# Kernel tuning notes

Measured on AMD Instinct MI355X. Metric: run time of the kernel, lower is better.

The kernel has to match this reference:

```python
import jax, jax.numpy as jnp
import numpy as np

HIDDEN = 768

def setup_inputs() -> dict:
    key = jax.random.key(0)
    k1, k2, k3 = jax.random.split(key, 3)
    x = jax.random.normal(k1, (8, 2048, HIDDEN), dtype=jnp.float32)
    # nn.Linear(hidden, 3*hidden): weight [3H, H], bias [3H]; torch init ~ U(-1/sqrt(H), 1/sqrt(H))
    bound = 1.0 / np.sqrt(HIDDEN)
    W = jax.random.uniform(k2, (3 * HIDDEN, HIDDEN), dtype=jnp.float32, minval=-bound, maxval=bound)
    b = jax.random.uniform(k3, (3 * HIDDEN,), dtype=jnp.float32, minval=-bound, maxval=bound)
    return {"x": x, "W": W, "b": b}

def reference(x, W, b):
    # qkv: [B, N, 3H]
    qkv = jnp.einsum('bnd,hd->bnh', x, W) + b
    q, k, v = jnp.split(qkv, 3, axis=-1)  # each [B, N, H]
    # NOTE: original module applies NO 1/sqrt(d) scaling — kept faithful.
    weights = jnp.einsum('bnd,bmd->bnm', q, k)          # [B, N, N]
    weights = jax.nn.softmax(weights, axis=-1)
    out = jnp.einsum('bnm,bmd->bnd', weights, v)        # [B, N, H]
    return out
```

## Files before the change

kernel.cpp:

```cpp
#include <hip/hip_runtime.h>


typedef short    s16x8 __attribute__((ext_vector_type(8)));
typedef _Float16 h16x8 __attribute__((ext_vector_type(8)));
typedef _Float16 h16x4 __attribute__((ext_vector_type(4)));
typedef float    f32x4 __attribute__((ext_vector_type(4)));

__device__ __forceinline__ unsigned short f2bf(float x) {
    unsigned u = __float_as_uint(x);
    u += 0x7fffu + ((u >> 16) & 1u);
    return (unsigned short)(u >> 16);
}
__device__ __forceinline__ float bf2f(unsigned short h) {
    return __uint_as_float(((unsigned)h) << 16);
}
__device__ __forceinline__ unsigned short f2h(float x) {
    _Float16 h = (_Float16)x;
    unsigned short u;
    __builtin_memcpy(&u, &h, 2);
    return u;
}

__device__ __forceinline__ void gld16(const void* g, void* l) {
    __builtin_amdgcn_global_load_lds(
        (const __attribute__((address_space(1))) unsigned int*)(unsigned long long)g,
        (__attribute__((address_space(3))) unsigned int*)(unsigned)(unsigned long long)l,
        16, 0, 0);
}

template<int MODE, bool FP16, int SWZ>
__global__ __launch_bounds__(256, 2)
void gemm_mfma(const unsigned short* __restrict__ A, const unsigned short* __restrict__ B,
               const float* __restrict__ bias, const float* __restrict__ rvec,
               float* __restrict__ Cf, unsigned short* __restrict__ Ch,
               int K, int lda, int ldb, int ldc,
               long long sA, long long sB, long long sC, long long sR)
{
    __shared__ unsigned short As[4096];
    __shared__ unsigned short Bs[4096];

    int bx = blockIdx.x, by = blockIdx.y, bz = blockIdx.z;
    if (SWZ == 1) {
        const int l = bx + gridDim.x * (by + gridDim.y * bz);
        bz = l & 7;
        const int t = l >> 3;
        bx = t % gridDim.x;
        by = t / gridDim.x;
    } else if (SWZ == 2) {
        const int l = bx + gridDim.x * by;
        const int c = l & 7;
        const int t = l >> 3;
        const int rows = gridDim.y >> 3;
        bx = t % gridDim.x;
        by = c * rows + t / gridDim.x;
    }

    A += (long long)bz * sA;
    B += (long long)bz * sB;

    const long long m0 = (long long)by * 128;
    const long long n0 = (long long)bx * 128;

    const int tid  = threadIdx.x;
    const int wave = tid >> 6, lane = tid & 63;
    const int rr_  = lane >> 2, kc = (lane & 3) * 8;
    const int wm = (wave & 1) * 64, wn = (wave >> 1) * 64;
    const int ml = lane & 15, kq = (lane >> 4) * 8;

    f32x4 acc[4][4];
#pragma unroll
    for (int i = 0; i < 4; ++i)
#pragma unroll
        for (int j = 0; j < 4; ++j) acc[i][j] = f32x4{0.f, 0.f, 0.f, 0.f};

    for (int kt = 0; kt < K; kt += 32) {
        __syncthreads();
#pragma unroll
        for (int i = 0; i < 2; ++i) {
            const int sc = wave * 2 + i;
            const long long ar = m0 + sc * 16 + rr_;
            const long long br = n0 + sc * 16 + rr_;
            gld16(A + ar * (long long)lda + kt + kc, As + sc * 512);
            gld16(B + br * (long long)ldb + kt + kc, Bs + sc * 512);
        }
        __syncthreads();

#pragma unroll
        for (int i = 0; i < 4; ++i) {
            const int ai = (wm + i * 16 + ml) * 32 + kq;
#pragma unroll
            for (int j = 0; j < 4; ++j) {
                const int bi = (wn + j * 16 + ml) * 32 + kq;
                if (FP16)
                    acc[i][j] = __builtin_amdgcn_mfma_f32_16x16x32_f16(
                        *(const h16x8*)&As[ai], *(const h16x8*)&Bs[bi], acc[i][j], 0, 0, 0);
                else
                    acc[i][j] = __builtin_amdgcn_mfma_f32_16x16x32_bf16(
                        *(const s16x8*)&As[ai], *(const s16x8*)&Bs[bi], acc[i][j], 0, 0, 0);
            }
        }
    }

    const int r0 = (lane >> 4) * 4;
    if (MODE == 1 || MODE == 2) {
#pragma unroll
        for (int i = 0; i < 4; ++i) {
            const long long rowb = m0 + wm + i * 16 + r0;
#pragma unroll
            for (int j = 0; j < 4; ++j) {
                const long long col = n0 + wn + j * 16 + ml;
                const float bj = bias[col];
#pragma unroll
                for (int q = 0; q < 4; ++q) {
                    const float v = acc[i][j][q] + bj;
                    Ch[(rowb + q) * (long long)ldc + col] = (MODE == 1) ? f2h(v) : f2bf(v);
                }
            }
        }
    } else if (MODE == 3) {
        Ch += (long long)bz * sC;
#pragma unroll
        for (int i = 0; i < 4; ++i) {
            const long long rowb = m0 + wm + i * 16 + r0;
#pragma unroll
            for (int j = 0; j < 4; ++j) {
                const long long col = n0 + wn + j * 16 + ml;
#pragma unroll
                for (int q = 0; q < 4; ++q)
                    Ch[(rowb + q) * (long long)ldc + col] = f2bf(__expf(acc[i][j][q]));
            }
        }
    } else {
        Cf += (long long)bz * sC;
        rvec += (long long)bz * sR;
#pragma unroll
        for (int i = 0; i < 4; ++i) {
            const long long rowb = m0 + wm + i * 16 + r0;
#pragma unroll
            for (int j = 0; j < 4; ++j) {
                const long long col = n0 + wn + j * 16 + ml;
#pragma unroll
                for (int q = 0; q < 4; ++q)
                    Cf[(rowb + q) * (long long)ldc + col] = acc[i][j][q] * rvec[rowb + q];
            }
        }
    }
}

__global__ __launch_bounds__(256)
void cvt_f16(const float* __restrict__ in, unsigned short* __restrict__ out, long long n4)
{
    const long long i = (long long)blockIdx.x * 256 + threadIdx.x;
    if (i >= n4) return;
    const float4 v = ((const float4*)in)[i];
    h16x4 o;
    o.x = (_Float16)v.x; o.y = (_Float16)v.y;
    o.z = (_Float16)v.z; o.w = (_Float16)v.w;
    ((h16x4*)out)[i] = o;
}

__global__ __launch_bounds__(256)
void transpose_v(const unsigned short* __restrict__ v, unsigned short* __restrict__ vt)
{
    __shared__ unsigned short t[32][33];
    const int b = blockIdx.z;
    const int n0 = blockIdx.x * 32, h0 = blockIdx.y * 32;
    const int tx = threadIdx.x, ty = threadIdx.y;
    const unsigned short* src = v + (long long)b * 2048 * 768;
#pragma unroll
    for (int q = 0; q < 4; ++q)
        t[ty + q * 8][tx] = src[(long long)(n0 + ty + q * 8) * 768 + h0 + tx];
    __syncthreads();
    unsigned short* dst = vt + ((long long)b * 768 + h0) * 2048 + n0;
#pragma unroll
    for (int q = 0; q < 4; ++q)
        dst[(long long)(ty + q * 8) * 2048 + tx] = t[tx][ty + q * 8];
}

__global__ __launch_bounds__(256)
void rowsum_recip(const unsigned short* __restrict__ E, float* __restrict__ r)
{
    const long long row = blockIdx.x;
    const int t = threadIdx.x, lane = t & 63, w = t >> 6;
    __shared__ float red[4];
    const uint4 v = ((const uint4*)(E + row * 2048))[t];
    float s = bf2f((unsigned short)(v.x & 0xffff)) + bf2f((unsigned short)(v.x >> 16))
            + bf2f((unsigned short)(v.y & 0xffff)) + bf2f((unsigned short)(v.y >> 16))
            + bf2f((unsigned short)(v.z & 0xffff)) + bf2f((unsigned short)(v.z >> 16))
            + bf2f((unsigned short)(v.w & 0xffff)) + bf2f((unsigned short)(v.w >> 16));
#pragma unroll
    for (int o = 32; o; o >>= 1) s += __shfl_xor(s, o);
    if (lane == 0) red[w] = s;
    __syncthreads();
    if (t == 0) r[row] = 1.f / ((red[0] + red[1]) + (red[2] + red[3]));
}

extern "C" void kernel_launch(void* const* d_in, const int* in_sizes, int n_in,
                              void* d_out, int out_size, void* d_ws, size_t ws_size,
                              hipStream_t stream)
{
    const float* x    = (const float*)d_in[0];
    const float* W    = (const float*)d_in[1];
    const float* bias = (const float*)d_in[2];
    float* out = (float*)d_out;

    char* ws = (char*)d_ws;
    unsigned short* xh = (unsigned short*)ws;
    unsigned short* Wh = (unsigned short*)(ws + 25165824LL);
    unsigned short* qk = (unsigned short*)(ws + 28704768LL);
    unsigned short* v  = (unsigned short*)(ws + 79036416LL);
    unsigned short* vt = (unsigned short*)(ws + 104202240LL);
    unsigned short* E  = (unsigned short*)(ws + 129368064LL);
    float*          r  = (float*)(ws + 196476928LL);

    cvt_f16<<<dim3(12288), dim3(256), 0, stream>>>(x, xh, 3145728LL);
    cvt_f16<<<dim3(1728),  dim3(256), 0, stream>>>(W, Wh, 442368LL);

    gemm_mfma<1, true, 2><<<dim3(12, 128, 1), dim3(256), 0, stream>>>(
        xh, Wh, bias, nullptr, nullptr, qk,
        768, 768, 768, 1536, 0, 0, 0, 0);

    gemm_mfma<2, true, 2><<<dim3(6, 128, 1), dim3(256), 0, stream>>>(
        xh, Wh + 1536LL * 768, bias + 1536, nullptr, nullptr, v,
        768, 768, 768, 768, 0, 0, 0, 0);

    transpose_v<<<dim3(64, 24, 8), dim3(32, 8), 0, stream>>>(v, vt);

    gemm_mfma<3, true, 1><<<dim3(16, 16, 8), dim3(256), 0, stream>>>(
        qk, qk + 768, nullptr, nullptr, nullptr, E,
        768, 1536, 1536, 2048,
        2048LL * 1536, 2048LL * 1536, 2048LL * 2048, 0);

    rowsum_recip<<<dim3(16384), dim3(256), 0, stream>>>(E, r);

    gemm_mfma<4, false, 1><<<dim3(6, 16, 8), dim3(256), 0, stream>>>(
        E, vt, nullptr, r, out, nullptr,
        2048, 2048, 2048, 768,
        2048LL * 2048, 768LL * 2048, 2048LL * 768, 2048);
}
```

Baseline: 341.5 us.

## Use 256x256 tiles with 8 waves and a 4-stage LDS prefetch pipeline

Rewrites the MFMA GEMM to compute a 256x256 output tile per 512-thread block, with each wave covering 128x64. Global-to-LDS loads go into a 4-deep ring buffer, prefetched three K-steps ahead, with explicit waitcnt and barriers so the loads overlap the MFMAs. s_setprio is raised around the MFMA bursts. The goal is more operand reuse per LDS load and hidden global latency, at the cost of 128KB of LDS per block and far fewer blocks in the grid, which risks low occupancy and tail underutilisation on the small projection GEMMs.

```diff
diff --git a/kernel.cpp b/kernel.cpp
--- a/kernel.cpp
+++ b/kernel.cpp
@@ -20,6 +20,9 @@
     __builtin_memcpy(&u, &h, 2);
     return u;
 }
+__device__ __forceinline__ h16x8 as_h(s16x8 v) {
+    h16x8 r; __builtin_memcpy(&r, &v, 16); return r;
+}
 
 __device__ __forceinline__ void gld16(const void* g, void* l) {
     __builtin_amdgcn_global_load_lds(
@@ -28,16 +31,24 @@
         16, 0, 0);
 }
 
+template<bool FP16>
+__device__ __forceinline__ f32x4 mma(s16x8 a, s16x8 b, f32x4 c) {
+    if constexpr (FP16)
+        return __builtin_amdgcn_mfma_f32_16x16x32_f16(as_h(a), as_h(b), c, 0, 0, 0);
+    else
+        return __builtin_amdgcn_mfma_f32_16x16x32_bf16(a, b, c, 0, 0, 0);
+}
+
 template<int MODE, bool FP16, int SWZ>
-__global__ __launch_bounds__(256, 2)
+__global__ __launch_bounds__(512, 2)
 void gemm_mfma(const unsigned short* __restrict__ A, const unsigned short* __restrict__ B,
                const float* __restrict__ bias, const float* __restrict__ rvec,
                float* __restrict__ Cf, unsigned short* __restrict__ Ch,
                int K, int lda, int ldb, int ldc,
                long long sA, long long sB, long long sC, long long sR)
 {
-    __shared__ unsigned short As[4096];
-    __shared__ unsigned short Bs[4096];
+    __shared__ unsigned short As[4][8192];
+    __shared__ unsigned short Bs[4][8192];
 
     int bx = blockIdx.x, by = blockIdx.y, bz = blockIdx.z;
     if (SWZ == 1) {
@@ -58,73 +69,119 @@
     A += (long long)bz * sA;
     B += (long long)bz * sB;
 
-    const long long m0 = (long long)by * 128;
-    const long long n0 = (long long)bx * 128;
+    const long long m0 = (long long)by * 256;
+    const long long n0 = (long long)bx * 256;
 
     const int tid  = threadIdx.x;
     const int wave = tid >> 6, lane = tid & 63;
-    const int rr_  = lane >> 2, kc = (lane & 3) * 8;
-    const int wm = (wave & 1) * 64, wn = (wave >> 1) * 64;
+    const int wr = wave >> 2, wc = wave & 3;
     const int ml = lane & 15, kq = (lane >> 4) * 8;
-
-    f32x4 acc[4][4];
-#pragma unroll
-    for (int i = 0; i < 4; ++i)
+    const int srr = wave * 16 + (lane >> 2);
+    const int skc = (lane & 3) * 8;
+
+    const int aidx = (wr * 128 + ml) * 32 + kq;
+    const int bidx = (wc * 64  + ml) * 32 + kq;
+
+    const unsigned short* Abase = A + (m0 + srr) * (long long)lda + skc;
+    const unsigned short* Bbase = B + (n0 + srr) * (long long)ldb + skc;
+    const long long a128 = 128LL * lda, b128 = 128LL * ldb;
+
+    auto stage_a = [&](int t, int buf) {
+        const unsigned short* p = Abase + t * 32;
+        gld16(p,        &As[buf][wave * 512]);
+        gld16(p + a128, &As[buf][4096 + wave * 512]);
+    };
+    auto stage_b = [&](int t, int buf) {
+        const unsigned short* p = Bbase + t * 32;
+        gld16(p,        &Bs[buf][wave * 512]);
+        gld16(p + b128, &Bs[buf][4096 + wave * 512]);
+    };
+
+    f32x4 acc[8][4];
+#pragma unroll
+    for (int i = 0; i < 8; ++i)
 #pragma unroll
         for (int j = 0; j < 4; ++j) acc[i][j] = f32x4{0.f, 0.f, 0.f, 0.f};
 
-    for (int kt = 0; kt < K; kt += 32) {
-        __syncthreads();
-#pragma unroll
-        for (int i = 0; i < 2; ++i) {
-            const int sc = wave * 2 + i;
-            const long long ar = m0 + sc * 16 + rr_;
-            const long long br = n0 + sc * 16 + rr_;
-            gld16(A + ar * (long long)lda + kt + kc, As + sc * 512);
-            gld16(B + br * (long long)ldb + kt + kc, Bs + sc * 512);
-        }
-        __syncthreads();
-
-#pragma unroll
-        for (int i = 0; i < 4; ++i) {
-            const int ai = (wm + i * 16 + ml) * 32 + kq;
+    const int nt = K >> 5;
+
+    stage_a(0, 0); stage_b(0, 0);
+    stage_a(1, 1); stage_b(1, 1);
+    stage_a(2, 2); stage_b(2, 2);
+    asm volatile("s_waitcnt vmcnt(8)");
+    __builtin_amdgcn_s_barrier();
+
+    for (int t = 0; t < nt; ++t) {
+        const int cur = t & 3;
+        const unsigned short* as = &As[cur][0];
+        const unsigned short* bs = &Bs[cur][0];
+        const bool pf = (t + 3 < nt);
+        const int nb = (t + 3) & 3;
+
+        s16x8 a4[4], b4[4];
+
+#pragma unroll
+        for (int i = 0; i < 4; ++i) a4[i] = *(const s16x8*)&as[aidx + i * 512];
+#pragma unroll
+        for (int j = 0; j < 4; ++j) b4[j] = *(const s16x8*)&bs[bidx + j * 512];
+        if (pf) stage_a(t + 3, nb);
+        __builtin_amdgcn_s_barrier();
+        asm volatile("s_waitcnt lgkmcnt(0)");
+        __builtin_amdgcn_sched_barrier(0);
+        __builtin_amdgcn_s_setprio(1);
+#pragma unroll
+        for (int i = 0; i < 4; ++i)
+#pragma unroll
+            for (int j = 0; j < 4; ++j)
+                acc[i][j] = mma<FP16>(a4[i], b4[j], acc[i][j]);
+        __builtin_amdgcn_s_setprio(0);
+        __builtin_amdgcn_s_barrier();
+
+#pragma unroll
+        for (int i = 0; i < 4; ++i) a4[i] = *(const s16x8*)&as[aidx + (i + 4) * 512];
+        if (pf) stage_b(t + 3, nb);
+        __builtin_amdgcn_s_barrier();
+        asm volatile("s_waitcnt lgkmcnt(0)");
+        __builtin_amdgcn_sched_barrier(0);
+        __builtin_amdgcn_s_setprio(1);
+#pragma unroll
+        for (int i = 0; i < 4; ++i)
+#pragma unroll
+            for (int j = 0; j < 4; ++j)
+                acc[i + 4][j] = mma<FP16>(a4[i], b4[j], acc[i + 4][j]);
+        __builtin_amdgcn_s_setprio(0);
+        if (pf)                { asm volatile("s_waitcnt vmcnt(8)"); }
+        else if (t + 3 == nt)  { asm volatile("s_waitcnt vmcnt(4)"); }
+        else if (t + 2 == nt)  { asm volatile("s_waitcnt vmcnt(0)"); }
+        __builtin_amdgcn_s_barrier();
+    }
+
+    const int r0 = (lane >> 4) * 4;
+    const long long rowbase = m0 + wr * 128 + r0;
+    const long long colbase = n0 + wc * 64 + ml;
+    if (MODE == 1 || MODE == 2) {
+#pragma unroll
+        for (int i = 0; i < 8; ++i) {
+            const long long rowb = rowbase + i * 16;
 #pragma unroll
             for (int j = 0; j < 4; ++j) {
-                const int bi = (wn + j * 16 + ml) * 32 + kq;
-                if (FP16)
-                    acc[i][j] = __builtin_amdgcn_mfma_f32_16x16x32_f16(
-                        *(const h16x8*)&As[ai], *(const h16x8*)&Bs[bi], acc[i][j], 0, 0, 0);
-                else
-                    acc[i][j] = __builtin_amdgcn_mfma_f32_16x16x32_bf16(
-                        *(const s16x8*)&As[ai], *(const s16x8*)&Bs[bi], acc[i][j], 0, 0, 0);
-            }
-        }
-    }
-
-    const int r0 = (lane >> 4) * 4;
-    if (MODE == 1 || MODE == 2) {
-#pragma unroll
-        for (int i = 0; i < 4; ++i) {
-            const long long rowb = m0 + wm + i * 16 + r0;
-#pragma unroll
-            for (int j = 0; j < 4; ++j) {
-                const long long col = n0 + wn + j * 16 + ml;
+                const long long col = colbase + j * 16;
                 const float bj = bias[col];
 #pragma unroll
                 for (int q = 0; q < 4; ++q) {
-                    const float v = acc[i][j][q] + bj;
-                    Ch[(rowb + q) * (long long)ldc + col] = (MODE == 1) ? f2h(v) : f2bf(v);
+                    const float vv = acc[i][j][q] + bj;
+                    Ch[(rowb + q) * (long long)ldc + col] = (MODE == 1) ? f2h(vv) : f2bf(vv);
                 }
             }
         }
     } else if (MODE == 3) {
         Ch += (long long)bz * sC;
 #pragma unroll
-        for (int i = 0; i < 4; ++i) {
-            const long long rowb = m0 + wm + i * 16 + r0;
+        for (int i = 0; i < 8; ++i) {
+            const long long rowb = rowbase + i * 16;
 #pragma unroll
             for (int j = 0; j < 4; ++j) {
-                const long long col = n0 + wn + j * 16 + ml;
+                const long long col = colbase + j * 16;
 #pragma unroll
                 for (int q = 0; q < 4; ++q)
                     Ch[(rowb + q) * (long long)ldc + col] = f2bf(__expf(acc[i][j][q]));
@@ -134,11 +191,11 @@
         Cf += (long long)bz * sC;
         rvec += (long long)bz * sR;
 #pragma unroll
-        for (int i = 0; i < 4; ++i) {
-            const long long rowb = m0 + wm + i * 16 + r0;
+        for (int i = 0; i < 8; ++i) {
+            const long long rowb = rowbase + i * 16;
 #pragma unroll
             for (int j = 0; j < 4; ++j) {
-                const long long col = n0 + wn + j * 16 + ml;
+                const long long col = colbase + j * 16;
 #pragma unroll
                 for (int q = 0; q < 4; ++q)
                     Cf[(rowb + q) * (long long)ldc + col] = acc[i][j][q] * rvec[rowb + q];
@@ -216,24 +273,24 @@
     cvt_f16<<<dim3(12288), dim3(256), 0, stream>>>(x, xh, 3145728LL);
     cvt_f16<<<dim3(1728),  dim3(256), 0, stream>>>(W, Wh, 442368LL);
 
-    gemm_mfma<1, true, 2><<<dim3(12, 128, 1), dim3(256), 0, stream>>>(
+    gemm_mfma<1, true, 2><<<dim3(6, 64, 1), dim3(512), 0, stream>>>(
         xh, Wh, bias, nullptr, nullptr, qk,
         768, 768, 768, 1536, 0, 0, 0, 0);
 
-    gemm_mfma<2, true, 2><<<dim3(6, 128, 1), dim3(256), 0, stream>>>(
+    gemm_mfma<2, true, 2><<<dim3(3, 64, 1), dim3(512), 0, stream>>>(
         xh, Wh + 1536LL * 768, bias + 1536, nullptr, nullptr, v,
         768, 768, 768, 768, 0, 0, 0, 0);
 
     transpose_v<<<dim3(64, 24, 8), dim3(32, 8), 0, stream>>>(v, vt);
 
-    gemm_mfma<3, true, 1><<<dim3(16, 16, 8), dim3(256), 0, stream>>>(
+    gemm_mfma<3, true, 1><<<dim3(8, 8, 8), dim3(512), 0, stream>>>(
         qk, qk + 768, nullptr, nullptr, nullptr, E,
         768, 1536, 1536, 2048,
         2048LL * 1536, 2048LL * 1536, 2048LL * 2048, 0);
 
     rowsum_recip<<<dim3(16384), dim3(256), 0, stream>>>(E, r);
 
-    gemm_mfma<4, false, 1><<<dim3(6, 16, 8), dim3(256), 0, stream>>>(
+    gemm_mfma<4, false, 1><<<dim3(3, 8, 8), dim3(512), 0, stream>>>(
         E, vt, nullptr, r, out, nullptr,
         2048, 2048, 2048, 768,
         2048LL * 2048, 768LL * 2048, 2048LL * 768, 2048);
```

New measurement: 350.4 us. +2.6%, slower.
